# Performance work log

Hardware: AMD Instinct MI355X
Metric: run time of the kernel (lower is better)

Reference implementation:

```python
import jax, jax.numpy as jnp
import numpy as np

N = 32768          # total nodes
B = 64             # number of graphs (batch.max()+1)
IN_C = 256
OUT_C = 256
NUM_SCALES = 4
NUM_HEADS = 8
BN_EPS = 1e-5


def setup_inputs() -> dict:
    key = jax.random.key(0)
    ks = jax.random.split(key, 10)
    out_s = OUT_C // NUM_SCALES
    x = jax.random.normal(ks[0], (N, IN_C), jnp.float32)
    spectral = jax.random.normal(ks[1], (NUM_SCALES, N, IN_C), jnp.float32)
    batch = jnp.sort(jax.random.randint(ks[2], (N,), 0, B)).astype(jnp.int64)
    # per-scale Linear weights (glorot) and zero biases; stored as [S, in, out_s]
    g = (6.0 / (IN_C + out_s)) ** 0.5
    Ws = jax.random.uniform(ks[3], (NUM_SCALES, IN_C, out_s), jnp.float32, -g, g)
    bs = jnp.zeros((NUM_SCALES, out_s), jnp.float32)
    # MultiheadAttention params (torch layout: in_proj [3E,E], out_proj [E,E])
    s_in = (1.0 / OUT_C) ** 0.5
    W_in = jax.random.uniform(ks[4], (3 * OUT_C, OUT_C), jnp.float32, -s_in, s_in)
    b_in = jnp.zeros((3 * OUT_C,), jnp.float32)
    W_out = jax.random.uniform(ks[5], (OUT_C, OUT_C), jnp.float32, -s_in, s_in)
    b_out = jnp.zeros((OUT_C,), jnp.float32)
    gamma = jnp.ones((OUT_C,), jnp.float32)
    beta = jnp.zeros((OUT_C,), jnp.float32)
    return {"x": x, "spectral": spectral, "Ws": Ws, "bs": bs,
            "W_in": W_in, "b_in": b_in, "W_out": W_out, "b_out": b_out,
            "gamma": gamma, "beta": beta, "batch": batch}


def _forward(x, spectral, Ws, bs, W_in, b_in, W_out, b_out, gamma, beta, batch):
    n, E = x.shape[0], W_out.shape[0]
    # per-scale linear on (x + spectral_feat), concat over scales -> [N, E]
    scale_out = jnp.einsum('sni,sio->sno', x[None] + spectral, Ws) + bs[:, None, :]
    h = jnp.moveaxis(scale_out, 0, 1).reshape(n, E)
    # ragged -> dense padding (batch is sorted segment ids)
    counts = jnp.bincount(batch, length=B)
    max_nodes = int(np.asarray(counts).max())  # data-dependent pad, as in torch
    starts = jnp.concatenate([jnp.zeros((1,), counts.dtype), jnp.cumsum(counts)[:-1]])
    pos = jnp.arange(n) - starts[batch]
    h_pad = jnp.zeros((B, max_nodes, E), h.dtype).at[batch, pos].set(h)
    # MHA over padded graphs (no key-padding mask, matching the source)
    hd = E // NUM_HEADS
    qkv = h_pad @ W_in.T + b_in                       # [B, M, 3E]
    q, k, v = jnp.split(qkv, 3, axis=-1)
    def heads(t):
        return t.reshape(B, max_nodes, NUM_HEADS, hd).transpose(0, 2, 1, 3)
    q, k, v = heads(q) * (hd ** -0.5), heads(k), heads(v)
    attn = jax.nn.softmax(jnp.einsum('bhqd,bhkd->bhqk', q, k), axis=-1)
    ctx = jnp.einsum('bhqk,bhkd->bhqd', attn, v)
    ctx = ctx.transpose(0, 2, 1, 3).reshape(B, max_nodes, E)
    h_att = ctx @ W_out.T + b_out
    # dense -> ragged unpad
    h2 = h_att[batch, pos]                            # [N, E]
    # BatchNorm1d (training-mode batch stats, deterministic) + ReLU; dropout=eval
    mean = h2.mean(axis=0)
    var = h2.var(axis=0)
    hn = (h2 - mean) * jax.lax.rsqrt(var + BN_EPS) * gamma + beta
    return jax.nn.relu(hn)


def reference(x, spectral, Ws, bs, W_in, b_in, W_out, b_out, gamma, beta, batch):
    return _forward(x, spectral, Ws, bs, W_in, b_in, W_out, b_out, gamma, beta, batch)
```

## Files before the change

### kernel.cpp

```cpp
#include <hip/hip_runtime.h>


typedef __attribute__((ext_vector_type(8))) short frag8;
typedef __attribute__((ext_vector_type(4))) short frag4;
typedef __attribute__((ext_vector_type(4))) float f32x4;
typedef __attribute__((ext_vector_type(8))) unsigned short ushort8;
typedef __attribute__((ext_vector_type(2))) unsigned int uint2e;

#define NN 32768
#define NB 64
#define CIN 256
#define COUT 256
#define NHEAD 8
#define HD 32

#define BM 128
#define LDB 264
#define KT 128

#if __has_builtin(__builtin_amdgcn_mfma_f32_16x16x16bf16_1k)
#define HAS_MFMA16 1
#else
#define HAS_MFMA16 0
#endif

#if __has_builtin(__builtin_amdgcn_exp2f)
#define EXP2(x) __builtin_amdgcn_exp2f(x)
#else
#define EXP2(x) __expf((x) * 0.6931471805599453f)
#endif

__device__ inline unsigned short f2bf(float f) {
  unsigned u = __builtin_bit_cast(unsigned, f);
  u += 0x7FFFu + ((u >> 16) & 1u);
  return (unsigned short)(u >> 16);
}
__device__ inline float bf2f(unsigned short h) {
  return __builtin_bit_cast(float, (unsigned)h << 16);
}
__device__ inline unsigned cvtpk(float a, float b) {
  unsigned r;
  asm("v_cvt_pk_bf16_f32 %0, %1, %2" : "=v"(r) : "v"(a), "v"(b));
  return r;
}

__global__ void k_prep(const float* __restrict__ Ws, const float* __restrict__ Win,
                       const float* __restrict__ Wout, const int* __restrict__ batch,
                       unsigned short* __restrict__ wst, unsigned short* __restrict__ winb,
                       unsigned short* __restrict__ woutb, int* __restrict__ meta) {
  int tid = blockIdx.x * 256 + threadIdx.x;
  if (tid < NN) {
    int v = batch[tid];
    int prev = (tid == 0) ? -1 : batch[tid - 1];
    for (int bb = prev + 1; bb <= v; ++bb) meta[NB + bb] = tid;
  }
  if (tid < 4 * 64 * 256) {
    int s = tid >> 14, rem = tid & 16383, o = rem >> 8, i = rem & 255;
    wst[tid] = f2bf(Ws[((s * 256) + i) * 64 + o]);
  } else if (tid < 4 * 64 * 256 + 768 * 256) {
    int t2 = tid - 4 * 64 * 256;
    winb[t2] = f2bf(Win[t2]);
  } else if (tid < 4 * 64 * 256 + 768 * 256 + 256 * 256) {
    int t3 = tid - (4 * 64 * 256 + 768 * 256);
    woutb[t3] = f2bf(Wout[t3]);
  }
}
__global__ void k_meta2(int* __restrict__ meta) {
  __shared__ int mx[NB];
  int b = threadIdx.x;
  int s = meta[NB + b];
  int e = (b == 63) ? NN : meta[NB + b + 1];
  meta[b] = e - s;
  mx[b] = e - s;
  __syncthreads();
  if (b == 0) {
    int m = 0;
    for (int j = 0; j < NB; ++j) m = max(m, mx[j]);
    meta[2 * NB] = m;
  }
}

__device__ inline void stage_Bpanel(const unsigned short* __restrict__ Wt,
                                    unsigned short (*Bs)[LDB], int t) {
  int n = t >> 2, seg = t & 3;
  const unsigned short* src = Wt + (size_t)n * 256 + seg * 64;
#pragma unroll
  for (int i = 0; i < 8; ++i) {
    uint4 v = *(const uint4*)(src + i * 8);
    *(uint4*)&Bs[n][seg * 64 + i * 8] = v;
  }
}


__global__ __launch_bounds__(256, 4) void k_scale(const float* __restrict__ x,
                                                  const float* __restrict__ spec,
                                                  const unsigned short* __restrict__ wst,
                                                  const float* __restrict__ bs,
                                                  unsigned short* __restrict__ h) {
  __shared__ unsigned short Bs[64][LDB];
  int bid = blockIdx.x;
  int bx = (bid & 7) * 32 + ((bid >> 3) & 31);
  int s = bid >> 8;
  int t = threadIdx.x, lane = t & 63, wave = t >> 6;
  int r0 = bx * BM;
  int m16 = lane & 15, quad = lane >> 4;

  stage_Bpanel(wst + (size_t)s * 64 * 256, Bs, t);

  const float* sb = spec + (size_t)s * NN * CIN;
  size_t rowbase0 = (size_t)(r0 + wave * 32 + m16) * CIN + quad * 8;
  const float* px0 = x + rowbase0;
  const float* px1 = px0 + 16 * CIN;
  const float* ps0 = sb + rowbase0;
  const float* ps1 = ps0 + 16 * CIN;

  float4 P[3][4];
#define ISSUE(slot, kc, mi)                                              \
  do {                                                                   \
    const float* px_ = (mi) ? px1 : px0;                                 \
    const float* ps_ = (mi) ? ps1 : ps0;                                 \
    P[(slot)][0] = *(const float4*)(px_ + (kc) * 32);                    \
    P[(slot)][1] = *(const float4*)(px_ + (kc) * 32 + 4);                \
    P[(slot)][2] = *(const float4*)(ps_ + (kc) * 32);                    \
    P[(slot)][3] = *(const float4*)(ps_ + (kc) * 32 + 4);                \
  } while (0)

  ISSUE(0, 0, 0);
  ISSUE(1, 0, 1);
  ISSUE(2, 1, 0);

  __syncthreads();

  f32x4 z = {0.f, 0.f, 0.f, 0.f};
  f32x4 acc[2][4];
#pragma unroll
  for (int mi = 0; mi < 2; ++mi)
#pragma unroll
    for (int ni = 0; ni < 4; ++ni) acc[mi][ni] = z;

#pragma unroll
  for (int st = 0; st < 16; ++st) {
    const int kc = st >> 1, mi = st & 1, slot = st % 3;
    uint4 u;
    u.x = cvtpk(P[slot][0].x + P[slot][2].x, P[slot][0].y + P[slot][2].y);
    u.y = cvtpk(P[slot][0].z + P[slot][2].z, P[slot][0].w + P[slot][2].w);
    u.z = cvtpk(P[slot][1].x + P[slot][3].x, P[slot][1].y + P[slot][3].y);
    u.w = cvtpk(P[slot][1].z + P[slot][3].z, P[slot][1].w + P[slot][3].w);
    frag8 a = __builtin_bit_cast(frag8, u);
    if (st + 3 < 16) ISSUE(slot, (st + 3) >> 1, (st + 3) & 1);
    frag8 b0 = *(const frag8*)&Bs[m16][kc * 32 + quad * 8];
    frag8 b1 = *(const frag8*)&Bs[16 + m16][kc * 32 + quad * 8];
    frag8 b2 = *(const frag8*)&Bs[32 + m16][kc * 32 + quad * 8];
    frag8 b3 = *(const frag8*)&Bs[48 + m16][kc * 32 + quad * 8];
    acc[mi][0] = __builtin_amdgcn_mfma_f32_16x16x32_bf16(a, b0, acc[mi][0], 0, 0, 0);
    acc[mi][1] = __builtin_amdgcn_mfma_f32_16x16x32_bf16(a, b1, acc[mi][1], 0, 0, 0);
    acc[mi][2] = __builtin_amdgcn_mfma_f32_16x16x32_bf16(a, b2, acc[mi][2], 0, 0, 0);
    acc[mi][3] = __builtin_amdgcn_mfma_f32_16x16x32_bf16(a, b3, acc[mi][3], 0, 0, 0);
  }
#undef ISSUE

#pragma unroll
  for (int mi = 0; mi < 2; ++mi)
#pragma unroll
    for (int ni = 0; ni < 4; ++ni) {
      int col = ni * 16 + m16;
      float bias = bs[s * 64 + col];
#pragma unroll
      for (int rp = 0; rp < 2; ++rp) {
        int row = r0 + wave * 32 + mi * 16 + quad * 4 + rp * 2;
        unsigned u = cvtpk(acc[mi][ni][rp * 2] + bias, acc[mi][ni][rp * 2 + 1] + bias);
        h[(size_t)row * COUT + s * 64 + col] = (unsigned short)u;
        h[(size_t)(row + 1) * COUT + s * 64 + col] = (unsigned short)(u >> 16);
      }
    }
}

template <int LDOUT, int NCB, bool DOSTATS>
__global__ __launch_bounds__(256, 4) void k_lin(const unsigned short* __restrict__ A,
                                                const unsigned short* __restrict__ Wt,
                                                const float* __restrict__ bias,
                                                unsigned short* __restrict__ out,
                                                float* __restrict__ sums) {
  __shared__ unsigned short Bs[64][LDB];
  int bid = blockIdx.x;
  int bx = (bid & 7) * 32 + ((bid >> 3) & 31);
  int cb = bid >> 8;
  int t = threadIdx.x, lane = t & 63, wave = t >> 6;
  int r0 = bx * BM, c0 = cb * 64;
  int m16 = lane & 15, quad = lane >> 4;

  stage_Bpanel(Wt + (size_t)c0 * 256, Bs, t);

  const unsigned short* pa0 = A + (size_t)(r0 + wave * 32 + m16) * 256 + quad * 8;
  const unsigned short* pa1 = pa0 + 16 * 256;

  frag8 PA[3];
  PA[0] = *(const frag8*)(pa0);
  PA[1] = *(const frag8*)(pa1);
  PA[2] = *(const frag8*)(pa0 + 32);

  __syncthreads();

  f32x4 z = {0.f, 0.f, 0.f, 0.f};
  f32x4 acc[2][4];
#pragma unroll
  for (int mi = 0; mi < 2; ++mi)
#pragma unroll
    for (int ni = 0; ni < 4; ++ni) acc[mi][ni] = z;

#pragma unroll
  for (int st = 0; st < 16; ++st) {
    const int kc = st >> 1, mi = st & 1, slot = st % 3;
    frag8 a = PA[slot];
    if (st + 3 < 16) {
      const int nst = st + 3;
      PA[slot] = *(const frag8*)(((nst & 1) ? pa1 : pa0) + (nst >> 1) * 32);
    }
    frag8 b0 = *(const frag8*)&Bs[m16][kc * 32 + quad * 8];
    frag8 b1 = *(const frag8*)&Bs[16 + m16][kc * 32 + quad * 8];
    frag8 b2 = *(const frag8*)&Bs[32 + m16][kc * 32 + quad * 8];
    frag8 b3 = *(const frag8*)&Bs[48 + m16][kc * 32 + quad * 8];
    acc[mi][0] = __builtin_amdgcn_mfma_f32_16x16x32_bf16(a, b0, acc[mi][0], 0, 0, 0);
    acc[mi][1] = __builtin_amdgcn_mfma_f32_16x16x32_bf16(a, b1, acc[mi][1], 0, 0, 0);
    acc[mi][2] = __builtin_amdgcn_mfma_f32_16x16x32_bf16(a, b2, acc[mi][2], 0, 0, 0);
    acc[mi][3] = __builtin_amdgcn_mfma_f32_16x16x32_bf16(a, b3, acc[mi][3], 0, 0, 0);
  }

#pragma unroll
  for (int ni = 0; ni < 4; ++ni) {
    int col = c0 + ni * 16 + m16;
    float bv = bias[col];
    float s1 = 0.f, s2 = 0.f;
#pragma unroll
    for (int mi = 0; mi < 2; ++mi) {
#pragma unroll
      for (int rp = 0; rp < 2; ++rp) {
        float v0 = acc[mi][ni][rp * 2] + bv;
        float v1 = acc[mi][ni][rp * 2 + 1] + bv;
        if (DOSTATS) { s1 += v0 + v1; s2 += v0 * v0 + v1 * v1; }
        int row = r0 + wave * 32 + mi * 16 + quad * 4 + rp * 2;
        unsigned u = cvtpk(v0, v1);
        out[(size_t)row * LDOUT + col] = (unsigned short)u;
        out[(size_t)(row + 1) * LDOUT + col] = (unsigned short)(u >> 16);
      }
    }
    if (DOSTATS) {
      s1 += __shfl_xor(s1, 16); s1 += __shfl_xor(s1, 32);
      s2 += __shfl_xor(s2, 16); s2 += __shfl_xor(s2, 32);
      if (quad == 0) {
        atomicAdd(&sums[col], s1);
        atomicAdd(&sums[256 + col], s2);
      }
    }
  }
}

__global__ __launch_bounds__(256) void k_attn_mfma(const unsigned short* __restrict__ qkv,
                                                   const int* __restrict__ meta,
                                                   unsigned short* __restrict__ ctx) {
  int bidx = blockIdx.x;
  int b = (bidx & 7) * 8 + ((bidx >> 3) & 7);
  int head = bidx >> 6;
  int c = meta[b], st = meta[NB + b], M = meta[2 * NB];
  int q0 = blockIdx.y * 128;
  if (q0 >= c) return;

  __shared__ unsigned short Vt[32][KT + 8];

  int t = threadIdx.x, lane = t & 63, wave = t >> 6;
  int m16 = lane & 15, quad = lane >> 4;
  const float SC2 = 0.17677669529663687f * 1.4426950408889634f;
  float extra = (float)(M - c);

  int qbase = q0 + wave * 32;
  frag8 qf[2];
#pragma unroll
  for (int qg = 0; qg < 2; ++qg) {
    int qrow = qbase + qg * 16 + m16;
    qf[qg] = *(const frag8*)(qkv + (size_t)(st + qrow) * 768 + head * 32 + quad * 8);
  }

  f32x4 zz = {0.f, 0.f, 0.f, 0.f};
  f32x4 O[2][2];
  float lp[2] = {0.f, 0.f};
#pragma unroll
  for (int qg = 0; qg < 2; ++qg) { O[qg][0] = zz; O[qg][1] = zz; }

#if !HAS_MFMA16
  int sl0 = m16 + ((quad & 1) << 5);
  int sl1 = sl0 + 16;
#endif

  for (int kt = 0; kt < c; kt += KT) {
    {
      int key = t >> 1, dh0 = (t & 1) * 16;
      const unsigned short* vp = qkv + (size_t)(st + kt + key) * 768 + 512 + head * 32 + dh0;
      ushort8 v0 = *(const ushort8*)vp;
      ushort8 v1 = *(const ushort8*)(vp + 8);
#pragma unroll
      for (int i = 0; i < 8; ++i) {
        Vt[dh0 + i][key] = v0[i];
        Vt[dh0 + 8 + i][key] = v1[i];
      }
    }
    __syncthreads();

#pragma unroll
    for (int sub = 0; sub < 4; ++sub) {
      int ks = kt + sub * 32;
      if (ks < c) {
        bool full = (ks + 32 <= c);
        frag8 kf[2];
#pragma unroll
        for (int kh = 0; kh < 2; ++kh) {
          int krow = ks + kh * 16 + m16;
          kf[kh] = *(const frag8*)(qkv + (size_t)(st + krow) * 768 + 256 + head * 32 + quad * 8);
        }
        unsigned pk[2][2][2];
#pragma unroll
        for (int qg = 0; qg < 2; ++qg)
#pragma unroll
          for (int kh = 0; kh < 2; ++kh) {
            f32x4 s = __builtin_amdgcn_mfma_f32_16x16x32_bf16(kf[kh], qf[qg], zz, 0, 0, 0);
            float p[4];
#pragma unroll
            for (int r = 0; r < 4; ++r) p[r] = EXP2(s[r] * SC2);
            if (!full) {
#pragma unroll
              for (int r = 0; r < 4; ++r)
                if (ks + kh * 16 + quad * 4 + r >= c) p[r] = 0.f;
            }
            lp[qg] += (p[0] + p[1]) + (p[2] + p[3]);
            pk[qg][kh][0] = cvtpk(p[0], p[1]);
            pk[qg][kh][1] = cvtpk(p[2], p[3]);
          }
#if HAS_MFMA16
        frag4 vb[2][2];
#pragma unroll
        for (int kh = 0; kh < 2; ++kh)
#pragma unroll
          for (int dh = 0; dh < 2; ++dh)
            vb[kh][dh] = *(const frag4*)&Vt[dh * 16 + m16][sub * 32 + kh * 16 + quad * 4];
#pragma unroll
        for (int qg = 0; qg < 2; ++qg) {
          frag4 pa0 = __builtin_bit_cast(frag4, uint2e{pk[qg][0][0], pk[qg][0][1]});
          frag4 pa1 = __builtin_bit_cast(frag4, uint2e{pk[qg][1][0], pk[qg][1][1]});
#pragma unroll
          for (int dh = 0; dh < 2; ++dh) {
            O[qg][dh] = __builtin_amdgcn_mfma_f32_16x16x16bf16_1k(pa0, vb[0][dh], O[qg][dh], 0, 0, 0);
            O[qg][dh] = __builtin_amdgcn_mfma_f32_16x16x16bf16_1k(pa1, vb[1][dh], O[qg][dh], 0, 0, 0);
          }
        }
#else
        frag8 vf[2];
#pragma unroll
        for (int dh = 0; dh < 2; ++dh)
          vf[dh] = *(const frag8*)&Vt[dh * 16 + m16][sub * 32 + quad * 8];
#pragma unroll
        for (int qg = 0; qg < 2; ++qg) {
          unsigned a0 = __shfl(pk[qg][0][0], sl0), a1 = __shfl(pk[qg][0][1], sl0);
          unsigned a2 = __shfl(pk[qg][0][0], sl1), a3 = __shfl(pk[qg][0][1], sl1);
          unsigned b0 = __shfl(pk[qg][1][0], sl0), b1 = __shfl(pk[qg][1][1], sl0);
          unsigned b2 = __shfl(pk[qg][1][0], sl1), b3 = __shfl(pk[qg][1][1], sl1);
          uint4 pw;
          pw.x = (quad < 2) ? a0 : b0;
          pw.y = (quad < 2) ? a1 : b1;
          pw.z = (quad < 2) ? a2 : b2;
          pw.w = (quad < 2) ? a3 : b3;
          frag8 pf = __builtin_bit_cast(frag8, pw);
#pragma unroll
          for (int dh = 0; dh < 2; ++dh)
            O[qg][dh] = __builtin_amdgcn_mfma_f32_16x16x32_bf16(pf, vf[dh], O[qg][dh], 0, 0, 0);
        }
#endif
      }
    }
    __syncthreads();
  }

#pragma unroll
  for (int qg = 0; qg < 2; ++qg) {
    float v = lp[qg];
    v += __shfl_xor(v, 16);
    v += __shfl_xor(v, 32);
    lp[qg] = v;
  }

#pragma unroll
  for (int qg = 0; qg < 2; ++qg)
#pragma unroll
    for (int r = 0; r < 4; ++r) {
      int qrow = qbase + qg * 16 + quad * 4 + r;
      float lsum = __shfl(lp[qg], quad * 4 + r);
      if (qrow < c) {
        float inv = 1.f / (lsum + extra);
        unsigned short* op = ctx + (size_t)(st + qrow) * 256 + head * 32;
        unsigned u = cvtpk(O[qg][0][r] * inv, O[qg][1][r] * inv);
        op[m16] = (unsigned short)u;
        op[16 + m16] = (unsigned short)(u >> 16);
      }
    }
}

__global__ __launch_bounds__(256) void k_bn_apply(const unsigned short* __restrict__ h,
                                                  const float* __restrict__ sums,
                                                  const float* __restrict__ gamma,
                                                  const float* __restrict__ beta,
                                                  float* __restrict__ out) {
  size_t i8 = ((size_t)blockIdx.x * 256 + threadIdx.x) * 8;
  int c0 = (int)(i8 & 255);
  ushort8 v = *(const ushort8*)(h + i8);
  float4 o0, o1;
  float res[8];
#pragma unroll
  for (int i = 0; i < 8; ++i) {
    int ch = c0 + i;
    float mean = sums[ch] * (1.0f / NN);
    float var = sums[256 + ch] * (1.0f / NN) - mean * mean;
    float sc = rsqrtf(var + 1e-5f) * gamma[ch];
    float sh = beta[ch] - mean * sc;
    res[i] = fmaxf(bf2f(v[i]) * sc + sh, 0.f);
  }
  o0.x = res[0]; o0.y = res[1]; o0.z = res[2]; o0.w = res[3];
  o1.x = res[4]; o1.y = res[5]; o1.z = res[6]; o1.w = res[7];
  *(float4*)(out + i8) = o0;
  *(float4*)(out + i8 + 4) = o1;
}

extern "C" void kernel_launch(void* const* d_in, const int* in_sizes, int n_in,
                              void* d_out, int out_size, void* d_ws, size_t ws_size,
                              hipStream_t stream) {
  const float* x      = (const float*)d_in[0];
  const float* spec   = (const float*)d_in[1];
  const float* Ws     = (const float*)d_in[2];
  const float* bs     = (const float*)d_in[3];
  const float* Win    = (const float*)d_in[4];
  const float* b_in   = (const float*)d_in[5];
  const float* Wout   = (const float*)d_in[6];
  const float* b_out  = (const float*)d_in[7];
  const float* gamma  = (const float*)d_in[8];
  const float* beta   = (const float*)d_in[9];
  const int* batch    = (const int*)d_in[10];
  float* out = (float*)d_out;

  char* w = (char*)d_ws;
  size_t off = 0;
  auto alloc = [&](size_t bytes) -> void* {
    off = (off + 255) & ~(size_t)255;
    void* p = w + off; off += bytes; return p;
  };
  int* meta             = (int*)alloc(129 * sizeof(int));
  unsigned short* wst   = (unsigned short*)alloc((size_t)4 * 64 * 256 * 2);
  unsigned short* winb  = (unsigned short*)alloc((size_t)768 * 256 * 2);
  unsigned short* woutb = (unsigned short*)alloc((size_t)256 * 256 * 2);
  float* sums           = (float*)alloc(512 * 4);
  unsigned short* h     = (unsigned short*)alloc((size_t)NN * 256 * 2);
  unsigned short* qkv   = (unsigned short*)alloc((size_t)NN * 768 * 2);
  unsigned short* ctx   = (unsigned short*)alloc((size_t)NN * 256 * 2);
  unsigned short* hatt  = (unsigned short*)alloc((size_t)NN * 256 * 2);

  (void)hipMemsetAsync(sums, 0, 512 * 4, stream);
  k_prep<<<1280, 256, 0, stream>>>(Ws, Win, Wout, batch, wst, winb, woutb, meta);
  k_meta2<<<1, 64, 0, stream>>>(meta);
  k_scale<<<NN / BM * 4, 256, 0, stream>>>(x, spec, wst, bs, h);
  k_lin<768, 12, false><<<NN / BM * 12, 256, 0, stream>>>(h, winb, b_in, qkv, nullptr);
  k_attn_mfma<<<dim3(NB * NHEAD, 8), 256, 0, stream>>>(qkv, meta, ctx);
  k_lin<256, 4, true><<<NN / BM * 4, 256, 0, stream>>>(ctx, woutb, b_out, hatt, sums);
  k_bn_apply<<<NN * 256 / 2048, 256, 0, stream>>>(hatt, sums, gamma, beta, out);
}
```

Baseline: 414.2 us.

## Stage x and spectral tiles into LDS via global_load_lds with swizzle

The scale GEMM now copies x and spectral tiles straight from global memory into a swizzled LDS chunk using global_load_lds, one K-chunk at a time. It then reads float4s from LDS to build the bf16 A fragments, replacing the register-prefetch pipeline. The goal is better coalesced, asynchronous loads of the dominant fp32 input stream. In exchange, each chunk now needs two barriers with no double buffering, and LDS use rises to about 66KB per block, which limits occupancy. The block-index swizzles in k_scale, k_lin and attention are also dropped in favour of plain 2D grids.

```diff
diff --git a/kernel.cpp b/kernel.cpp
--- a/kernel.cpp
+++ b/kernel.cpp
@@ -30,6 +30,12 @@
 #define EXP2(x) __expf((x) * 0.6931471805599453f)
 #endif
 
+#if __has_builtin(__builtin_amdgcn_global_load_lds)
+#define HAS_GLDS 1
+#else
+#define HAS_GLDS 0
+#endif
+
 __device__ inline unsigned short f2bf(float f) {
   unsigned u = __builtin_bit_cast(unsigned, f);
   u += 0x7FFFu + ((u >> 16) & 1u);
@@ -42,6 +48,17 @@
   unsigned r;
   asm("v_cvt_pk_bf16_f32 %0, %1, %2" : "=v"(r) : "v"(a), "v"(b));
   return r;
+}
+
+__device__ inline void gld16(const void* g, void* l) {
+#if HAS_GLDS
+  __builtin_amdgcn_global_load_lds(
+      (const __attribute__((address_space(1))) unsigned int*)g,
+      (__attribute__((address_space(3))) unsigned int*)l, 16, 0, 0);
+#else
+  int lane = threadIdx.x & 63;
+  *(float4*)((char*)l + lane * 16) = *(const float4*)g;
+#endif
 }
 
 __global__ void k_prep(const float* __restrict__ Ws, const float* __restrict__ Win,
@@ -92,43 +109,36 @@
 }
 
 
-__global__ __launch_bounds__(256, 4) void k_scale(const float* __restrict__ x,
-                                                  const float* __restrict__ spec,
-                                                  const unsigned short* __restrict__ wst,
-                                                  const float* __restrict__ bs,
-                                                  unsigned short* __restrict__ h) {
+__device__ inline void stage_chunk(const float* __restrict__ x,
+                                   const float* __restrict__ sb,
+                                   int r0, int kc, char* chunk, int t) {
+  int w = t >> 6, lane = t & 63;
+  const float* src = (w < 2) ? x : sb;
+  char* base = chunk + (w >> 1) * 16384 + (w & 1) * 8192;
+  int rlow = lane >> 3;
+  int slot = lane & 7;
+  int cswz = (slot ^ (rlow & 7)) << 2;
+  const float* g0 = src + (size_t)(r0 + (w & 1) * 64 + rlow) * CIN + kc * 32 + cswz;
+#pragma unroll
+  for (int j = 0; j < 8; ++j)
+    gld16(g0 + (size_t)j * 8 * CIN, base + j * 1024);
+}
+
+__global__ __launch_bounds__(256) void k_scale(const float* __restrict__ x,
+                                               const float* __restrict__ spec,
+                                               const unsigned short* __restrict__ wst,
+                                               const float* __restrict__ bs,
+                                               unsigned short* __restrict__ h) {
   __shared__ unsigned short Bs[64][LDB];
-  int bid = blockIdx.x;
-  int bx = (bid & 7) * 32 + ((bid >> 3) & 31);
-  int s = bid >> 8;
+  __shared__ __align__(16) char chunk[32768];
   int t = threadIdx.x, lane = t & 63, wave = t >> 6;
-  int r0 = bx * BM;
+  int r0 = blockIdx.x * BM, s = blockIdx.y;
   int m16 = lane & 15, quad = lane >> 4;
 
+  const float* sbp = spec + (size_t)s * NN * CIN;
+
   stage_Bpanel(wst + (size_t)s * 64 * 256, Bs, t);
-
-  const float* sb = spec + (size_t)s * NN * CIN;
-  size_t rowbase0 = (size_t)(r0 + wave * 32 + m16) * CIN + quad * 8;
-  const float* px0 = x + rowbase0;
-  const float* px1 = px0 + 16 * CIN;
-  const float* ps0 = sb + rowbase0;
-  const float* ps1 = ps0 + 16 * CIN;
-
-  float4 P[3][4];
-#define ISSUE(slot, kc, mi)                                              \
-  do {                                                                   \
-    const float* px_ = (mi) ? px1 : px0;                                 \
-    const float* ps_ = (mi) ? ps1 : ps0;                                 \
-    P[(slot)][0] = *(const float4*)(px_ + (kc) * 32);                    \
-    P[(slot)][1] = *(const float4*)(px_ + (kc) * 32 + 4);                \
-    P[(slot)][2] = *(const float4*)(ps_ + (kc) * 32);                    \
-    P[(slot)][3] = *(const float4*)(ps_ + (kc) * 32 + 4);                \
-  } while (0)
-
-  ISSUE(0, 0, 0);
-  ISSUE(1, 0, 1);
-  ISSUE(2, 1, 0);
-
+  stage_chunk(x, sbp, r0, 0, chunk, t);
   __syncthreads();
 
   f32x4 z = {0.f, 0.f, 0.f, 0.f};
@@ -138,16 +148,97 @@
 #pragma unroll
     for (int ni = 0; ni < 4; ++ni) acc[mi][ni] = z;
 
+  const char* xls = chunk;
+  const char* sls = chunk + 16384;
+  int sw = m16 & 7;
+  int s0 = (((quad << 1)) ^ sw) << 4;
+  int s1 = (((quad << 1) | 1) ^ sw) << 4;
+
+#pragma unroll
+  for (int kc = 0; kc < 8; ++kc) {
+#pragma unroll
+    for (int mi = 0; mi < 2; ++mi) {
+      int rb = (wave * 32 + mi * 16 + m16) << 7;
+      float4 xlo = *(const float4*)(xls + rb + s0);
+      float4 xhi = *(const float4*)(xls + rb + s1);
+      float4 plo = *(const float4*)(sls + rb + s0);
+      float4 phi = *(const float4*)(sls + rb + s1);
+      uint4 u;
+      u.x = cvtpk(xlo.x + plo.x, xlo.y + plo.y);
+      u.y = cvtpk(xlo.z + plo.z, xlo.w + plo.w);
+      u.z = cvtpk(xhi.x + phi.x, xhi.y + phi.y);
+      u.w = cvtpk(xhi.z + phi.z, xhi.w + phi.w);
+      frag8 a = __builtin_bit_cast(frag8, u);
+      frag8 b0 = *(const frag8*)&Bs[m16][kc * 32 + quad * 8];
+      frag8 b1 = *(const frag8*)&Bs[16 + m16][kc * 32 + quad * 8];
+      frag8 b2 = *(const frag8*)&Bs[32 + m16][kc * 32 + quad * 8];
+      frag8 b3 = *(const frag8*)&Bs[48 + m16][kc * 32 + quad * 8];
+      acc[mi][0] = __builtin_amdgcn_mfma_f32_16x16x32_bf16(a, b0, acc[mi][0], 0, 0, 0);
+      acc[mi][1] = __builtin_amdgcn_mfma_f32_16x16x32_bf16(a, b1, acc[mi][1], 0, 0, 0);
+      acc[mi][2] = __builtin_amdgcn_mfma_f32_16x16x32_bf16(a, b2, acc[mi][2], 0, 0, 0);
+      acc[mi][3] = __builtin_amdgcn_mfma_f32_16x16x32_bf16(a, b3, acc[mi][3], 0, 0, 0);
+    }
+    __syncthreads();
+    if (kc < 7) {
+      stage_chunk(x, sbp, r0, kc + 1, chunk, t);
+      __syncthreads();
+    }
+  }
+
+#pragma unroll
+  for (int mi = 0; mi < 2; ++mi)
+#pragma unroll
+    for (int ni = 0; ni < 4; ++ni) {
+      int col = ni * 16 + m16;
+      float bias = bs[s * 64 + col];
+#pragma unroll
+      for (int rp = 0; rp < 2; ++rp) {
+        int row = r0 + wave * 32 + mi * 16 + quad * 4 + rp * 2;
+        unsigned u = cvtpk(acc[mi][ni][rp * 2] + bias, acc[mi][ni][rp * 2 + 1] + bias);
+        h[(size_t)row * COUT + s * 64 + col] = (unsigned short)u;
+        h[(size_t)(row + 1) * COUT + s * 64 + col] = (unsigned short)(u >> 16);
+      }
+    }
+}
+
+template <int LDOUT, bool DOSTATS>
+__global__ __launch_bounds__(256, 4) void k_lin(const unsigned short* __restrict__ A,
+                                                const unsigned short* __restrict__ Wt,
+                                                const float* __restrict__ bias,
+                                                unsigned short* __restrict__ out,
+                                                float* __restrict__ sums) {
+  __shared__ unsigned short Bs[64][LDB];
+  int t = threadIdx.x, lane = t & 63, wave = t >> 6;
+  int r0 = blockIdx.x * BM, c0 = blockIdx.y * 64;
+  int m16 = lane & 15, quad = lane >> 4;
+
+  stage_Bpanel(Wt + (size_t)c0 * 256, Bs, t);
+
+  const unsigned short* pa0 = A + (size_t)(r0 + wave * 32 + m16) * 256 + quad * 8;
+  const unsigned short* pa1 = pa0 + 16 * 256;
+
+  frag8 PA[3];
+  PA[0] = *(const frag8*)(pa0);
+  PA[1] = *(const frag8*)(pa1);
+  PA[2] = *(const frag8*)(pa0 + 32);
+
+  __syncthreads();
+
+  f32x4 z = {0.f, 0.f, 0.f, 0.f};
+  f32x4 acc[2][4];
+#pragma unroll
+  for (int mi = 0; mi < 2; ++mi)
+#pragma unroll
+    for (int ni = 0; ni < 4; ++ni) acc[mi][ni] = z;
+
 #pragma unroll
   for (int st = 0; st < 16; ++st) {
     const int kc = st >> 1, mi = st & 1, slot = st % 3;
-    uint4 u;
-    u.x = cvtpk(P[slot][0].x + P[slot][2].x, P[slot][0].y + P[slot][2].y);
-    u.y = cvtpk(P[slot][0].z + P[slot][2].z, P[slot][0].w + P[slot][2].w);
-    u.z = cvtpk(P[slot][1].x + P[slot][3].x, P[slot][1].y + P[slot][3].y);
-    u.w = cvtpk(P[slot][1].z + P[slot][3].z, P[slot][1].w + P[slot][3].w);
-    frag8 a = __builtin_bit_cast(frag8, u);
-    if (st + 3 < 16) ISSUE(slot, (st + 3) >> 1, (st + 3) & 1);
+    frag8 a = PA[slot];
+    if (st + 3 < 16) {
+      const int nst = st + 3;
+      PA[slot] = *(const frag8*)(((nst & 1) ? pa1 : pa0) + (nst >> 1) * 32);
+    }
     frag8 b0 = *(const frag8*)&Bs[m16][kc * 32 + quad * 8];
     frag8 b1 = *(const frag8*)&Bs[16 + m16][kc * 32 + quad * 8];
     frag8 b2 = *(const frag8*)&Bs[32 + m16][kc * 32 + quad * 8];
@@ -157,74 +248,6 @@
     acc[mi][2] = __builtin_amdgcn_mfma_f32_16x16x32_bf16(a, b2, acc[mi][2], 0, 0, 0);
     acc[mi][3] = __builtin_amdgcn_mfma_f32_16x16x32_bf16(a, b3, acc[mi][3], 0, 0, 0);
   }
-#undef ISSUE
-
-#pragma unroll
-  for (int mi = 0; mi < 2; ++mi)
-#pragma unroll
-    for (int ni = 0; ni < 4; ++ni) {
-      int col = ni * 16 + m16;
-      float bias = bs[s * 64 + col];
-#pragma unroll
-      for (int rp = 0; rp < 2; ++rp) {
-        int row = r0 + wave * 32 + mi * 16 + quad * 4 + rp * 2;
-        unsigned u = cvtpk(acc[mi][ni][rp * 2] + bias, acc[mi][ni][rp * 2 + 1] + bias);
-        h[(size_t)row * COUT + s * 64 + col] = (unsigned short)u;
-        h[(size_t)(row + 1) * COUT + s * 64 + col] = (unsigned short)(u >> 16);
-      }
-    }
-}
-
-template <int LDOUT, int NCB, bool DOSTATS>
-__global__ __launch_bounds__(256, 4) void k_lin(const unsigned short* __restrict__ A,
-                                                const unsigned short* __restrict__ Wt,
-                                                const float* __restrict__ bias,
-                                                unsigned short* __restrict__ out,
-                                                float* __restrict__ sums) {
-  __shared__ unsigned short Bs[64][LDB];
-  int bid = blockIdx.x;
-  int bx = (bid & 7) * 32 + ((bid >> 3) & 31);
-  int cb = bid >> 8;
-  int t = threadIdx.x, lane = t & 63, wave = t >> 6;
-  int r0 = bx * BM, c0 = cb * 64;
-  int m16 = lane & 15, quad = lane >> 4;
-
-  stage_Bpanel(Wt + (size_t)c0 * 256, Bs, t);
-
-  const unsigned short* pa0 = A + (size_t)(r0 + wave * 32 + m16) * 256 + quad * 8;
-  const unsigned short* pa1 = pa0 + 16 * 256;
-
-  frag8 PA[3];
-  PA[0] = *(const frag8*)(pa0);
-  PA[1] = *(const frag8*)(pa1);
-  PA[2] = *(const frag8*)(pa0 + 32);
-
-  __syncthreads();
-
-  f32x4 z = {0.f, 0.f, 0.f, 0.f};
-  f32x4 acc[2][4];
-#pragma unroll
-  for (int mi = 0; mi < 2; ++mi)
-#pragma unroll
-    for (int ni = 0; ni < 4; ++ni) acc[mi][ni] = z;
-
-#pragma unroll
-  for (int st = 0; st < 16; ++st) {
-    const int kc = st >> 1, mi = st & 1, slot = st % 3;
-    frag8 a = PA[slot];
-    if (st + 3 < 16) {
-      const int nst = st + 3;
-      PA[slot] = *(const frag8*)(((nst & 1) ? pa1 : pa0) + (nst >> 1) * 32);
-    }
-    frag8 b0 = *(const frag8*)&Bs[m16][kc * 32 + quad * 8];
-    frag8 b1 = *(const frag8*)&Bs[16 + m16][kc * 32 + quad * 8];
-    frag8 b2 = *(const frag8*)&Bs[32 + m16][kc * 32 + quad * 8];
-    frag8 b3 = *(const frag8*)&Bs[48 + m16][kc * 32 + quad * 8];
-    acc[mi][0] = __builtin_amdgcn_mfma_f32_16x16x32_bf16(a, b0, acc[mi][0], 0, 0, 0);
-    acc[mi][1] = __builtin_amdgcn_mfma_f32_16x16x32_bf16(a, b1, acc[mi][1], 0, 0, 0);
-    acc[mi][2] = __builtin_amdgcn_mfma_f32_16x16x32_bf16(a, b2, acc[mi][2], 0, 0, 0);
-    acc[mi][3] = __builtin_amdgcn_mfma_f32_16x16x32_bf16(a, b3, acc[mi][3], 0, 0, 0);
-  }
 
 #pragma unroll
   for (int ni = 0; ni < 4; ++ni) {
@@ -258,9 +281,7 @@
 __global__ __launch_bounds__(256) void k_attn_mfma(const unsigned short* __restrict__ qkv,
                                                    const int* __restrict__ meta,
                                                    unsigned short* __restrict__ ctx) {
-  int bidx = blockIdx.x;
-  int b = (bidx & 7) * 8 + ((bidx >> 3) & 7);
-  int head = bidx >> 6;
+  int b = blockIdx.x >> 3, head = blockIdx.x & 7;
   int c = meta[b], st = meta[NB + b], M = meta[2 * NB];
   int q0 = blockIdx.y * 128;
   if (q0 >= c) return;
@@ -462,9 +483,9 @@
   (void)hipMemsetAsync(sums, 0, 512 * 4, stream);
   k_prep<<<1280, 256, 0, stream>>>(Ws, Win, Wout, batch, wst, winb, woutb, meta);
   k_meta2<<<1, 64, 0, stream>>>(meta);
-  k_scale<<<NN / BM * 4, 256, 0, stream>>>(x, spec, wst, bs, h);
-  k_lin<768, 12, false><<<NN / BM * 12, 256, 0, stream>>>(h, winb, b_in, qkv, nullptr);
+  k_scale<<<dim3(NN / BM, 4), 256, 0, stream>>>(x, spec, wst, bs, h);
+  k_lin<768, false><<<dim3(NN / BM, 12), 256, 0, stream>>>(h, winb, b_in, qkv, nullptr);
   k_attn_mfma<<<dim3(NB * NHEAD, 8), 256, 0, stream>>>(qkv, meta, ctx);
-  k_lin<256, 4, true><<<NN / BM * 4, 256, 0, stream>>>(ctx, woutb, b_out, hatt, sums);
+  k_lin<256, true><<<dim3(NN / BM, 4), 256, 0, stream>>>(ctx, woutb, b_out, hatt, sums);
   k_bn_apply<<<NN * 256 / 2048, 256, 0, stream>>>(hatt, sums, gamma, beta, out);
 }
```

New measurement: 419.0 us. Within noise of the previous version (+1.2%).
